# Performance work log

Hardware: AMD Instinct MI355X
Metric: run time of the kernel (lower is better)

## Reference

```python
import jax, jax.numpy as jnp
import numpy as np

B, S, HID = 2, 2048, 2048
NH, NKV, HD = 16, 4, 128  # num_heads, num_kv_heads, head_dim; kqv_size = NH*HD = 2048
KV_DIM = NKV * HD  # 512


def setup_inputs() -> dict:
    key = jax.random.key(0)
    ks = jax.random.split(key, 7)
    sc = 0.02
    return {
        "hidden_states": jax.random.normal(ks[0], (B, S, HID), dtype=jnp.float32),
        "Wq": jax.random.normal(ks[1], (NH * HD, HID), dtype=jnp.float32) * sc,
        "Wk": jax.random.normal(ks[2], (KV_DIM, HID), dtype=jnp.float32) * sc,
        "Wv": jax.random.normal(ks[3], (KV_DIM, HID), dtype=jnp.float32) * sc,
        "Wo": jax.random.normal(ks[4], (HID, NH * HD), dtype=jnp.float32) * sc,
        "bo": jnp.zeros((HID,), dtype=jnp.float32),
    }


def reference(hidden_states, Wq, Wk, Wv, Wo, bo):
    b, s, _ = hidden_states.shape
    # projections (nn.Linear: x @ W.T), no bias on q/k/v
    q = (hidden_states @ Wq.T).reshape(b, s, NH, HD).transpose(0, 2, 1, 3)   # [B,NH,S,HD]
    k = (hidden_states @ Wk.T).reshape(b, s, NKV, HD).transpose(0, 2, 1, 3)  # [B,NKV,S,HD]
    v = (hidden_states @ Wv.T).reshape(b, s, NKV, HD).transpose(0, 2, 1, 3)
    # GQA: query head h uses kv head h // (NH // NKV)
    g = NH // NKV
    k_rep = jnp.repeat(k, g, axis=1)  # [B,NH,S,HD]
    v_rep = jnp.repeat(v, g, axis=1)
    # float32 upcast, NO 1/sqrt(d) scaling (GPT-Neo style)
    qf = q.astype(jnp.float32)
    kf = k_rep.astype(jnp.float32)
    scores = jnp.einsum("bhqd,bhkd->bhqk", qf, kf)  # [B,NH,S,S]
    causal = jnp.tril(jnp.ones((s, s), dtype=bool))[None, None]
    neg = jnp.finfo(scores.dtype).min
    scores = jnp.where(causal, scores, neg)
    attn = jax.nn.softmax(scores, axis=-1).astype(v.dtype)  # dropout p=0 (eval)
    out = jnp.einsum("bhqk,bhkd->bhqd", attn, v_rep)         # [B,NH,S,HD]
    out = out.transpose(0, 2, 1, 3).reshape(b, s, NH * HD)
    return out @ Wo.T + bo
```

## Files before the change

### kernel.cpp

```cpp
#include <hip/hip_runtime.h>

typedef _Float16 f16;
typedef __attribute__((ext_vector_type(4))) _Float16 f16x4;
typedef __attribute__((ext_vector_type(8))) _Float16 f16x8;
typedef __attribute__((ext_vector_type(4))) float f32x4;

#define NB 2
#define NS 2048
#define NHID 2048
#define N_H 16
#define N_KV 4
#define N_HD 128

__device__ __forceinline__ void gload16(void* lds, const void* g) {
  __builtin_amdgcn_global_load_lds(
      (const __attribute__((address_space(1))) unsigned int*)g,
      (__attribute__((address_space(3))) unsigned int*)lds, 16, 0, 0);
}

__global__ __launch_bounds__(256) void cvt_all(
    const float* __restrict__ hs, const float* __restrict__ Wq,
    const float* __restrict__ Wk, const float* __restrict__ Wv,
    const float* __restrict__ Wo, f16* __restrict__ Xh,
    f16* __restrict__ Wqkv, f16* __restrict__ Woh) {
  int i = blockIdx.x * 256 + threadIdx.x;
  const float* src;
  f16* dst;
  int j;
  if (i < 2097152)      { src = hs; dst = Xh;             j = i; }
  else if (i < 3145728) { src = Wq; dst = Wqkv;           j = i - 2097152; }
  else if (i < 3407872) { src = Wk; dst = Wqkv + 4194304; j = i - 3145728; }
  else if (i < 3670016) { src = Wv; dst = Wqkv + 5242880; j = i - 3407872; }
  else                  { src = Wo; dst = Woh;            j = i - 3670016; }
  const float4 v = reinterpret_cast<const float4*>(src)[j];
  f16x4 o = {(f16)v.x, (f16)v.y, (f16)v.z, (f16)v.w};
  reinterpret_cast<f16x4*>(dst)[j] = o;
}

__global__ __launch_bounds__(512, 2) void gemm_qkv(
    const f16* __restrict__ A, const f16* __restrict__ Bm,
    f16* __restrict__ q_out, f16* __restrict__ k_out, f16* __restrict__ v_out) {
  constexpr int K = 2048;
  __shared__ f16 lds[2][28672];
  const int t = threadIdx.x;
  const int l = t & 63, w = t >> 6;
  const int g = l >> 4, l15 = l & 15;
  const int wr = w >> 2, wc = w & 3;
  const int orig = blockIdx.x;
  const int x = orig & 7, loc = orig >> 3;
  const int mb = (x & 3) * 4 + (loc & 3);
  const int nb = (x >> 2) * 8 + (loc >> 2);
  const f16* Ab = A + (size_t)(mb * 256) * K;
  const f16* Bb = Bm + (size_t)(nb * 192) * K;

  const int rA = ((t >> 5) << 3) | (t & 7);
  const int cA = (t >> 3) & 3;
  const int t2 = t & 255;
  const int rB2 = ((t2 >> 5) << 3) | (t2 & 7);
  const int cB2 = (t2 >> 3) & 3;

  auto stage = [&](int kt) {
    f16* buf = lds[kt & 1];
#pragma unroll
    for (int h = 0; h < 2; ++h) {
#pragma unroll
      for (int gi = 0; gi < 2; ++gi)
        gload16(buf + h * 8192 + gi * 4096 + w * 512,
                Ab + (size_t)(gi * 128 + rA) * K + kt * 64 + h * 32 + cA * 8);
      gload16(buf + 16384 + h * 6144 + w * 512,
              Bb + (size_t)rA * K + kt * 64 + h * 32 + cA * 8);
      if (t < 256)
        gload16(buf + 16384 + h * 6144 + 4096 + w * 512,
                Bb + (size_t)(128 + rB2) * K + kt * 64 + h * 32 + cB2 * 8);
    }
  };
  const int fragoff = ((l15 >> 3) << 8) + (g << 6) + ((l15 & 7) << 3);

  f32x4 acc[8][3] = {};

  stage(0);
  asm volatile("s_waitcnt vmcnt(0)" ::: "memory");
  __builtin_amdgcn_s_barrier();

  for (int kt = 0; kt < 32; ++kt) {
    if (kt + 1 < 32) stage(kt + 1);
    const f16* buf = lds[kt & 1];
#pragma unroll
    for (int h = 0; h < 2; ++h) {
      f16x8 af[8], bf[3];
#pragma unroll
      for (int mi = 0; mi < 8; ++mi)
        af[mi] = *reinterpret_cast<const f16x8*>(buf + h * 8192 + (wr * 128 + mi * 16) * 32 + fragoff);
#pragma unroll
      for (int ni = 0; ni < 3; ++ni)
        bf[ni] = *reinterpret_cast<const f16x8*>(buf + 16384 + h * 6144 + (wc * 48 + ni * 16) * 32 + fragoff);
      __builtin_amdgcn_s_setprio(1);
#pragma unroll
      for (int mi = 0; mi < 8; ++mi)
#pragma unroll
        for (int ni = 0; ni < 3; ++ni)
          acc[mi][ni] = __builtin_amdgcn_mfma_f32_16x16x32_f16(af[mi], bf[ni], acc[mi][ni], 0, 0, 0);
      __builtin_amdgcn_s_setprio(0);
    }
    if (kt + 1 < 32) asm volatile("s_waitcnt vmcnt(0)" ::: "memory");
    __builtin_amdgcn_s_barrier();
  }

#pragma unroll
  for (int mi = 0; mi < 8; ++mi) {
    int m0 = mb * 256 + wr * 128 + mi * 16 + 4 * g;
#pragma unroll
    for (int ni = 0; ni < 3; ++ni) {
      int n = nb * 192 + wc * 48 + ni * 16 + l15;
#pragma unroll
      for (int r = 0; r < 4; ++r) {
        int mm = m0 + r;
        float val = acc[mi][ni][r];
        int b = mm >> 11, s = mm & (NS - 1);
        if (n < 2048) {
          int h = n >> 7, d = n & 127;
          q_out[(((size_t)(b * N_H + h)) * NS + s) * N_HD + d] = (f16)val;
        } else if (n < 2560) {
          int n2 = n - 2048, kvh = n2 >> 7, d = n2 & 127;
          k_out[(((size_t)(b * N_KV + kvh)) * NS + s) * N_HD + d] = (f16)val;
        } else {
          int n3 = n - 2560, kvh = n3 >> 7, d = n3 & 127;
          v_out[(((size_t)(b * N_KV + kvh)) * NS + s) * N_HD + d] = (f16)val;
        }
      }
    }
  }
}

template <int MREP, int MODE>
__global__ __launch_bounds__(512, 2) void gemm8(
    const f16* __restrict__ A, const f16* __restrict__ Bm, const int K,
    float* __restrict__ f_out, const float* __restrict__ bias) {
  constexpr int BM = MREP * 32;
  constexpr int GA = BM / 128;
  constexpr int G = GA + 2;
  constexpr int NPH = (MREP == 8) ? 2 : 1;
  constexpr int ATILE = BM * 32;
  constexpr int BTILE = 256 * 32;
  constexpr int BUF = ATILE + BTILE;
  __shared__ f16 lds[4 * BUF];

  const int t = threadIdx.x;
  const int l = t & 63, w = t >> 6;
  const int g = l >> 4, l15 = l & 15;
  const int wr = w >> 2, wc = w & 3;
  const int orig = blockIdx.x;
  const int x = orig & 7, loc = orig >> 3;
  int mb, nb;
  mb = (x & 3) * 8 + (loc & 7); nb = (x >> 2) * 4 + (loc >> 3);
  const int NT = K >> 5;

  const f16* Aorig = A + (size_t)(mb * BM) * K;
  const f16* Borig = Bm + (size_t)(nb * 256) * K;

  size_t offA[GA], offB[2];
#pragma unroll
  for (int gi = 0; gi < GA; ++gi) {
    int beta = gi * 8192 + t * 16;
    int r = ((beta >> 9) << 3) | ((beta >> 4) & 7);
    int c = (beta >> 7) & 3;
    offA[gi] = (size_t)r * K + c * 8;
  }
#pragma unroll
  for (int gj = 0; gj < 2; ++gj) {
    int beta = gj * 8192 + t * 16;
    int r = ((beta >> 9) << 3) | ((beta >> 4) & 7);
    int c = (beta >> 7) & 3;
    offB[gj] = (size_t)r * K + c * 8;
  }

  auto stage = [&](int kt, int gi) {
    f16* bufbase = lds + (kt & 3) * BUF;
    if (gi < GA) {
      gload16(bufbase + gi * 4096 + w * 512, Aorig + offA[gi] + kt * 32);
    } else {
      int gj = gi - GA;
      gload16(bufbase + ATILE + gj * 4096 + w * 512, Borig + offB[gj] + kt * 32);
    }
  };
  const int fragoff = ((l15 >> 3) << 8) + (g << 6) + ((l15 & 7) << 3);
  auto readA = [&](int kt, int mi) -> f16x8 {
    int R0 = wr * (MREP * 16) + mi * 16;
    return *reinterpret_cast<const f16x8*>(lds + (kt & 3) * BUF + R0 * 32 + fragoff);
  };
  auto readB = [&](int kt, int ni) -> f16x8 {
    int R0 = wc * 64 + ni * 16;
    return *reinterpret_cast<const f16x8*>(lds + (kt & 3) * BUF + ATILE + R0 * 32 + fragoff);
  };

  f32x4 acc[MREP][4] = {};

#pragma unroll
  for (int pt = 0; pt < 3; ++pt)
#pragma unroll
    for (int gi = 0; gi < G; ++gi) stage(pt, gi);
  asm volatile("s_waitcnt vmcnt(6)" ::: "memory");
  __builtin_amdgcn_s_barrier();

  f16x8 bf[4];
  for (int kt = 0; kt < NT; ++kt) {
    const bool dostage = (kt + 3 < NT);
#pragma unroll
    for (int ph = 0; ph < NPH; ++ph) {
      f16x8 af[4];
#pragma unroll
      for (int mi = 0; mi < 4; ++mi) af[mi] = readA(kt, ph * 4 + mi);
      if (ph == 0) {
#pragma unroll
        for (int ni = 0; ni < 4; ++ni) bf[ni] = readB(kt, ni);
      }
      if (dostage) {
        stage(kt + 3, 0);
        stage(kt + 3, 1);
        stage(kt + 3, 2);
      }
      if (ph == NPH - 1) {
        if (kt + 3 < NT)      asm volatile("s_waitcnt vmcnt(6)" ::: "memory");
        else if (kt + 2 < NT) asm volatile("s_waitcnt vmcnt(3)" ::: "memory");
        else if (kt + 1 < NT) asm volatile("s_waitcnt vmcnt(0)" ::: "memory");
      }
      __builtin_amdgcn_s_barrier();
      asm volatile("s_waitcnt lgkmcnt(0)" ::: "memory");
      __builtin_amdgcn_s_setprio(1);
#pragma unroll
      for (int mi = 0; mi < 4; ++mi)
#pragma unroll
        for (int ni = 0; ni < 4; ++ni)
          acc[ph * 4 + mi][ni] =
              __builtin_amdgcn_mfma_f32_16x16x32_f16(af[mi], bf[ni], acc[ph * 4 + mi][ni], 0, 0, 0);
      __builtin_amdgcn_s_setprio(0);
      __builtin_amdgcn_s_barrier();
    }
  }

#pragma unroll
  for (int mi = 0; mi < MREP; ++mi) {
    int m0 = mb * BM + wr * (MREP * 16) + mi * 16 + 4 * g;
#pragma unroll
    for (int ni = 0; ni < 4; ++ni) {
      int n = nb * 256 + wc * 64 + ni * 16 + l15;
#pragma unroll
      for (int r = 0; r < 4; ++r) {
        f_out[(size_t)(m0 + r) * NHID + n] = acc[mi][ni][r] + bias[n];
      }
    }
  }
}

__global__ __launch_bounds__(256) void transpose_v(const f16* __restrict__ V,
                                                   f16* __restrict__ Vt) {
  __shared__ f16 tt[64][72];
  int s0 = blockIdx.x * 64, d0 = blockIdx.y * 64, bk = blockIdx.z;
  const f16* Vp = V + (size_t)bk * NS * N_HD;
  f16* Vtp = Vt + (size_t)bk * N_HD * NS;
  int tid = threadIdx.x;
#pragma unroll
  for (int it = 0; it < 2; ++it) {
    int c = it * 256 + tid;
    int sr = c >> 3, dc = (c & 7) * 8;
    f16x8 v = *reinterpret_cast<const f16x8*>(Vp + (size_t)(s0 + sr) * N_HD + d0 + dc);
#pragma unroll
    for (int j = 0; j < 8; ++j) tt[dc + j][sr] = v[j];
  }
  __syncthreads();
#pragma unroll
  for (int it = 0; it < 2; ++it) {
    int c = it * 256 + tid;
    int dr = c >> 3, sc = (c & 7) * 8;
    f16x8 o;
#pragma unroll
    for (int j = 0; j < 8; ++j) o[j] = tt[dr][sc + j];
    *reinterpret_cast<f16x8*>(Vtp + (size_t)(d0 + dr) * NS + s0 + sc) = o;
  }
}

__device__ __forceinline__ void stage_kv(const f16* __restrict__ Kp,
                                         const f16* __restrict__ Vp,
                                         f16* Kl, f16* Vl, int kt, int w, int l) {
#pragma unroll
  for (int it = 0; it < 4; ++it) {
    int cb = (it * 4 + w) * 64;
    int c = cb + l;
    int krow = c >> 4, pch = c & 15;
    int sch = (pch & 8) | ((pch ^ krow) & 7);
    gload16(Kl + cb * 8, Kp + (size_t)(kt * 64 + krow) * N_HD + sch * 8);
  }
#pragma unroll
  for (int it = 0; it < 4; ++it) {
    int cb = (it * 4 + w) * 64;
    int c = cb + l;
    int drow = c >> 3, pch = c & 7;
    int sch = (pch ^ drow) & 7;
    gload16(Vl + cb * 8, Vp + (size_t)drow * NS + kt * 64 + sch * 8);
  }
}

__device__ __forceinline__ void attn_step(
    const f16x8* qf, f32x4* oacc, float* mrow, float* lrow, int q0, int kt,
    const f16* Kl, const f16* Vl, f16* Pw, int g, int l15, bool diag) {
  f32x4 sacc[4];
#pragma unroll
  for (int nt = 0; nt < 4; ++nt) {
    f32x4 z = {0.f, 0.f, 0.f, 0.f};
#pragma unroll
    for (int ks = 0; ks < 4; ++ks) {
      int kr = nt * 16 + l15;
      int ch = ks * 4 + g;
      int sw = (ch & 8) | ((ch ^ kr) & 7);
      f16x8 kf = *reinterpret_cast<const f16x8*>(Kl + kr * 128 + sw * 8);
      z = __builtin_amdgcn_mfma_f32_16x16x32_f16(qf[ks], kf, z, 0, 0, 0);
    }
    sacc[nt] = z;
  }

  float p[4][4];
#pragma unroll
  for (int r = 0; r < 4; ++r) {
    int qg = q0 + r;
    float m = -3.0e38f;
#pragma unroll
    for (int nt = 0; nt < 4; ++nt) {
      float sv = sacc[nt][r];
      if (diag) {
        int kg = kt * 64 + nt * 16 + l15;
        if (kg > qg) sv = -3.0e38f;
      }
      p[nt][r] = sv;
      m = fmaxf(m, sv);
    }
#pragma unroll
    for (int off = 8; off >= 1; off >>= 1) m = fmaxf(m, __shfl_xor(m, off));
    float m2 = fmaxf(mrow[r], m);
    float alpha = __builtin_amdgcn_exp2f(mrow[r] - m2);
    mrow[r] = m2;
    lrow[r] *= alpha;
#pragma unroll
    for (int nt = 0; nt < 4; ++nt)
      p[nt][r] = __builtin_amdgcn_exp2f(p[nt][r] - m2);
#pragma unroll
    for (int dt = 0; dt < 8; ++dt) oacc[dt][r] *= alpha;
  }

#pragma unroll
  for (int nt = 0; nt < 4; ++nt)
#pragma unroll
    for (int r = 0; r < 4; ++r) {
      int ql = 4 * g + r;
      int kp = nt * 16 + l15;
      int ch = kp >> 3;
      int idx = ql * 64 + (ch ^ (ql & 7)) * 8 + (kp & 7);
      Pw[idx] = (f16)p[nt][r];
    }
  asm volatile("s_waitcnt lgkmcnt(0)" ::: "memory");
  __builtin_amdgcn_sched_barrier(0);

  f16x8 pa[2];
#pragma unroll
  for (int ks2 = 0; ks2 < 2; ++ks2) {
    int ch = ks2 * 4 + g;
    pa[ks2] = *reinterpret_cast<const f16x8*>(&Pw[l15 * 64 + (ch ^ (l15 & 7)) * 8]);
  }
  const f16x8 ones = {(f16)1.f, (f16)1.f, (f16)1.f, (f16)1.f,
                      (f16)1.f, (f16)1.f, (f16)1.f, (f16)1.f};
  f32x4 lacc = {0.f, 0.f, 0.f, 0.f};
#pragma unroll
  for (int ks2 = 0; ks2 < 2; ++ks2)
    lacc = __builtin_amdgcn_mfma_f32_16x16x32_f16(pa[ks2], ones, lacc, 0, 0, 0);
#pragma unroll
  for (int dt = 0; dt < 8; ++dt)
#pragma unroll
    for (int ks2 = 0; ks2 < 2; ++ks2) {
      int d = dt * 16 + l15;
      int ch = ks2 * 4 + g;
      f16x8 vf = *reinterpret_cast<const f16x8*>(Vl + d * 64 + (ch ^ (d & 7)) * 8);
      oacc[dt] = __builtin_amdgcn_mfma_f32_16x16x32_f16(pa[ks2], vf, oacc[dt], 0, 0, 0);
    }
#pragma unroll
  for (int r = 0; r < 4; ++r) lrow[r] += lacc[r];
}

__global__ __launch_bounds__(256, 2) void attn_kernel(
    const f16* __restrict__ Q, const f16* __restrict__ K,
    const f16* __restrict__ Vt, f16* __restrict__ O) {
  __shared__ f16 Klds[2][64 * 128];
  __shared__ f16 Vlds[2][128 * 64];
  __shared__ f16 Plds[4][16 * 64];
  const int t = threadIdx.x, l = t & 63, w = t >> 6;
  const int g = l >> 4, l15 = l & 15;
  const int orig = blockIdx.x;
  const int x = orig & 7, loc = orig >> 3;
  const int b = x >> 2, kvh = x & 3;
  const int h = kvh * 4 + (loc & 3);
  const int pi = loc >> 2;
  const int qtA = pi, qtB = 31 - pi;
  const f16* Qp = Q + ((size_t)(b * N_H + h)) * NS * N_HD;
  const f16* Kp = K + ((size_t)(b * N_KV + kvh)) * NS * N_HD;
  const f16* Vp = Vt + ((size_t)(b * N_KV + kvh)) * N_HD * NS;

  const f16 l2e = (f16)1.44269504f;
  f16x8 qfA[4], qfB[4];
  const int qrA = qtA * 64 + w * 16 + l15;
  const int qrB = qtB * 64 + w * 16 + l15;
#pragma unroll
  for (int ks = 0; ks < 4; ++ks) {
    qfA[ks] = *reinterpret_cast<const f16x8*>(Qp + (size_t)qrA * N_HD + ks * 32 + g * 8);
    qfB[ks] = *reinterpret_cast<const f16x8*>(Qp + (size_t)qrB * N_HD + ks * 32 + g * 8);
#pragma unroll
    for (int j = 0; j < 8; ++j) { qfA[ks][j] *= l2e; qfB[ks][j] *= l2e; }
  }

  f32x4 oA[8] = {}, oB[8] = {};
  float mA[4], lAr[4], mB[4], lBr[4];
#pragma unroll
  for (int r = 0; r < 4; ++r) {
    mA[r] = -3.0e38f; lAr[r] = 0.f;
    mB[r] = -3.0e38f; lBr[r] = 0.f;
  }
  const int q0A = qtA * 64 + w * 16 + 4 * g;
  const int q0B = qtB * 64 + w * 16 + 4 * g;

  const int nkt = qtB + 1;
  stage_kv(Kp, Vp, Klds[0], Vlds[0], 0, w, l);
  asm volatile("s_waitcnt vmcnt(0)" ::: "memory");
  __syncthreads();
  int cur = 0;
  for (int kt = 0; kt < nkt; ++kt) {
    if (kt + 1 < nkt)
      stage_kv(Kp, Vp, Klds[cur ^ 1], Vlds[cur ^ 1], kt + 1, w, l);
    attn_step(qfB, oB, mB, lBr, q0B, kt, Klds[cur], Vlds[cur], Plds[w], g, l15, kt == qtB);
    if (kt <= qtA)
      attn_step(qfA, oA, mA, lAr, q0A, kt, Klds[cur], Vlds[cur], Plds[w], g, l15, kt == qtA);
    asm volatile("s_waitcnt vmcnt(0)" ::: "memory");
    __syncthreads();
    cur ^= 1;
  }

#pragma unroll
  for (int r = 0; r < 4; ++r) {
    float invB = 1.0f / lBr[r];
    f16* orowB = O + (size_t)(b * NS + q0B + r) * NHID + h * N_HD;
#pragma unroll
    for (int dt = 0; dt < 8; ++dt) orowB[dt * 16 + l15] = (f16)(oB[dt][r] * invB);
    float invA = 1.0f / lAr[r];
    f16* orowA = O + (size_t)(b * NS + q0A + r) * NHID + h * N_HD;
#pragma unroll
    for (int dt = 0; dt < 8; ++dt) orowA[dt * 16 + l15] = (f16)(oA[dt][r] * invA);
  }
}

extern "C" void kernel_launch(void* const* d_in, const int* in_sizes, int n_in,
                              void* d_out, int out_size, void* d_ws, size_t ws_size,
                              hipStream_t stream) {
  const float* hs = (const float*)d_in[0];
  const float* Wq = (const float*)d_in[1];
  const float* Wk = (const float*)d_in[2];
  const float* Wv = (const float*)d_in[3];
  const float* Wo = (const float*)d_in[4];
  const float* bo = (const float*)d_in[5];
  float* out = (float*)d_out;

  char* ws = (char*)d_ws;
  f16* Xh   = (f16*)(ws);
  f16* Wqkv = (f16*)(ws + 16777216);
  f16* Woh  = (f16*)(ws + 29360128);
  f16* Qb   = (f16*)(ws + 37748736);
  f16* Kb   = (f16*)(ws + 54525952);
  f16* Vb   = (f16*)(ws + 58720256);
  f16* Vtb  = (f16*)(ws + 62914560);
  f16* Ob   = Xh;

  cvt_all<<<18432, 256, 0, stream>>>(hs, Wq, Wk, Wv, Wo, Xh, Wqkv, Woh);
  gemm_qkv<<<256, 512, 0, stream>>>(Xh, Wqkv, Qb, Kb, Vb);
  transpose_v<<<dim3(32, 2, 8), 256, 0, stream>>>(Vb, Vtb);
  attn_kernel<<<512, 256, 0, stream>>>(Qb, Kb, Vtb, Ob);
  gemm8<4, 1><<<256, 512, 0, stream>>>(Ob, Woh, 2048, out, bo);
}
```

Baseline: 216.1 us.

## Compute transposed attention scores to keep P in registers, skipping LDS round-trip

The attention step now computes S^T (K as the A operand, Q as B), so each lane owns one query row. The probabilities can then feed the PV MFMA directly as 16x16x16 B operands without being staged through LDS. This removes the per-step P write/read to shared memory, the lgkmcnt wait and the row-max shuffles, and simplifies the row statistics to scalars. The QKV GEMM also staggers which k-half each wave reads first to spread LDS bank traffic, and the output GEMM drops its unused multi-phase path. The trade-off is smaller 16x16x16 MFMAs and f16x4 V reads in place of the wider x32 instructions.

```diff
diff --git a/kernel.cpp b/kernel.cpp
--- a/kernel.cpp
+++ b/kernel.cpp
@@ -86,7 +86,8 @@
     if (kt + 1 < 32) stage(kt + 1);
     const f16* buf = lds[kt & 1];
 #pragma unroll
-    for (int h = 0; h < 2; ++h) {
+    for (int hi = 0; hi < 2; ++hi) {
+      const int h = hi ^ (w & 1);
       f16x8 af[8], bf[3];
 #pragma unroll
       for (int mi = 0; mi < 8; ++mi)
@@ -132,14 +133,13 @@
   }
 }
 
-template <int MREP, int MODE>
+template <int MREP>
 __global__ __launch_bounds__(512, 2) void gemm8(
     const f16* __restrict__ A, const f16* __restrict__ Bm, const int K,
     float* __restrict__ f_out, const float* __restrict__ bias) {
   constexpr int BM = MREP * 32;
   constexpr int GA = BM / 128;
   constexpr int G = GA + 2;
-  constexpr int NPH = (MREP == 8) ? 2 : 1;
   constexpr int ATILE = BM * 32;
   constexpr int BTILE = 256 * 32;
   constexpr int BUF = ATILE + BTILE;
@@ -151,8 +151,8 @@
   const int wr = w >> 2, wc = w & 3;
   const int orig = blockIdx.x;
   const int x = orig & 7, loc = orig >> 3;
-  int mb, nb;
-  mb = (x & 3) * 8 + (loc & 7); nb = (x >> 2) * 4 + (loc >> 3);
+  const int mb = (x & 3) * 8 + (loc & 7);
+  const int nb = (x >> 2) * 4 + (loc >> 3);
   const int NT = K >> 5;
 
   const f16* Aorig = A + (size_t)(mb * BM) * K;
@@ -202,40 +202,32 @@
   asm volatile("s_waitcnt vmcnt(6)" ::: "memory");
   __builtin_amdgcn_s_barrier();
 
-  f16x8 bf[4];
   for (int kt = 0; kt < NT; ++kt) {
-    const bool dostage = (kt + 3 < NT);
-#pragma unroll
-    for (int ph = 0; ph < NPH; ++ph) {
-      f16x8 af[4];
-#pragma unroll
-      for (int mi = 0; mi < 4; ++mi) af[mi] = readA(kt, ph * 4 + mi);
-      if (ph == 0) {
-#pragma unroll
-        for (int ni = 0; ni < 4; ++ni) bf[ni] = readB(kt, ni);
-      }
-      if (dostage) {
-        stage(kt + 3, 0);
-        stage(kt + 3, 1);
-        stage(kt + 3, 2);
-      }
-      if (ph == NPH - 1) {
-        if (kt + 3 < NT)      asm volatile("s_waitcnt vmcnt(6)" ::: "memory");
-        else if (kt + 2 < NT) asm volatile("s_waitcnt vmcnt(3)" ::: "memory");
-        else if (kt + 1 < NT) asm volatile("s_waitcnt vmcnt(0)" ::: "memory");
-      }
-      __builtin_amdgcn_s_barrier();
-      asm volatile("s_waitcnt lgkmcnt(0)" ::: "memory");
-      __builtin_amdgcn_s_setprio(1);
-#pragma unroll
-      for (int mi = 0; mi < 4; ++mi)
-#pragma unroll
-        for (int ni = 0; ni < 4; ++ni)
-          acc[ph * 4 + mi][ni] =
-              __builtin_amdgcn_mfma_f32_16x16x32_f16(af[mi], bf[ni], acc[ph * 4 + mi][ni], 0, 0, 0);
-      __builtin_amdgcn_s_setprio(0);
-      __builtin_amdgcn_s_barrier();
-    }
+    f16x8 af[4], bf[4];
+#pragma unroll
+    for (int mi = 0; mi < 4; ++mi) af[mi] = readA(kt, mi);
+#pragma unroll
+    for (int ni = 0; ni < 4; ++ni) bf[ni] = readB(kt, ni);
+    if (kt + 3 < NT) {
+      stage(kt + 3, 0);
+      stage(kt + 3, 1);
+      stage(kt + 3, 2);
+      asm volatile("s_waitcnt vmcnt(6)" ::: "memory");
+    } else if (kt + 2 < NT) {
+      asm volatile("s_waitcnt vmcnt(3)" ::: "memory");
+    } else if (kt + 1 < NT) {
+      asm volatile("s_waitcnt vmcnt(0)" ::: "memory");
+    }
+    __builtin_amdgcn_s_barrier();
+    asm volatile("s_waitcnt lgkmcnt(0)" ::: "memory");
+    __builtin_amdgcn_s_setprio(1);
+#pragma unroll
+    for (int mi = 0; mi < 4; ++mi)
+#pragma unroll
+      for (int ni = 0; ni < 4; ++ni)
+        acc[mi][ni] = __builtin_amdgcn_mfma_f32_16x16x32_f16(af[mi], bf[ni], acc[mi][ni], 0, 0, 0);
+    __builtin_amdgcn_s_setprio(0);
+    __builtin_amdgcn_s_barrier();
   }
 
 #pragma unroll
@@ -245,9 +237,8 @@
     for (int ni = 0; ni < 4; ++ni) {
       int n = nb * 256 + wc * 64 + ni * 16 + l15;
 #pragma unroll
-      for (int r = 0; r < 4; ++r) {
+      for (int r = 0; r < 4; ++r)
         f_out[(size_t)(m0 + r) * NHID + n] = acc[mi][ni][r] + bias[n];
-      }
     }
   }
 }
@@ -301,8 +292,8 @@
 }
 
 __device__ __forceinline__ void attn_step(
-    const f16x8* qf, f32x4* oacc, float* mrow, float* lrow, int q0, int kt,
-    const f16* Kl, const f16* Vl, f16* Pw, int g, int l15, bool diag) {
+    const f16x8* qf, f32x4* oacc, float& mrow, float& lrow, int qg, int kbase,
+    const f16* Kl, const f16* Vl, int g, int l15, bool diag) {
   f32x4 sacc[4];
 #pragma unroll
   for (int nt = 0; nt < 4; ++nt) {
@@ -313,75 +304,62 @@
       int ch = ks * 4 + g;
       int sw = (ch & 8) | ((ch ^ kr) & 7);
       f16x8 kf = *reinterpret_cast<const f16x8*>(Kl + kr * 128 + sw * 8);
-      z = __builtin_amdgcn_mfma_f32_16x16x32_f16(qf[ks], kf, z, 0, 0, 0);
+      z = __builtin_amdgcn_mfma_f32_16x16x32_f16(kf, qf[ks], z, 0, 0, 0);
     }
     sacc[nt] = z;
   }
 
-  float p[4][4];
-#pragma unroll
-  for (int r = 0; r < 4; ++r) {
-    int qg = q0 + r;
-    float m = -3.0e38f;
+  float pm[4][4];
+  float m = -3.0e38f;
+#pragma unroll
+  for (int nt = 0; nt < 4; ++nt)
+#pragma unroll
+    for (int r = 0; r < 4; ++r) {
+      float sv = sacc[nt][r];
+      if (diag && (kbase + nt * 16 + 4 * g + r > qg)) sv = -3.0e38f;
+      pm[nt][r] = sv;
+      m = fmaxf(m, sv);
+    }
+  m = fmaxf(m, __shfl_xor(m, 16));
+  m = fmaxf(m, __shfl_xor(m, 32));
+  float m2 = fmaxf(mrow, m);
+  float alpha = __builtin_amdgcn_exp2f(mrow - m2);
+  mrow = m2;
+
+  f16x4 p4[4];
+#pragma unroll
+  for (int nt = 0; nt < 4; ++nt) {
+    f16x4 q4 = {(f16)__builtin_amdgcn_exp2f(pm[nt][0] - m2),
+                (f16)__builtin_amdgcn_exp2f(pm[nt][1] - m2),
+                (f16)__builtin_amdgcn_exp2f(pm[nt][2] - m2),
+                (f16)__builtin_amdgcn_exp2f(pm[nt][3] - m2)};
+    p4[nt] = q4;
+  }
+
+  const f16x4 ones = {(f16)1.f, (f16)1.f, (f16)1.f, (f16)1.f};
+  f32x4 lacc = {0.f, 0.f, 0.f, 0.f};
+#pragma unroll
+  for (int nt = 0; nt < 4; ++nt)
+    lacc = __builtin_amdgcn_mfma_f32_16x16x16f16(ones, p4[nt], lacc, 0, 0, 0);
+  lrow = lrow * alpha + lacc[0];
+
+#pragma unroll
+  for (int dt = 0; dt < 8; ++dt) {
+    oacc[dt][0] *= alpha; oacc[dt][1] *= alpha;
+    oacc[dt][2] *= alpha; oacc[dt][3] *= alpha;
+  }
+
+#pragma unroll
+  for (int dt = 0; dt < 8; ++dt) {
+    int d = dt * 16 + l15;
 #pragma unroll
     for (int nt = 0; nt < 4; ++nt) {
-      float sv = sacc[nt][r];
-      if (diag) {
-        int kg = kt * 64 + nt * 16 + l15;
-        if (kg > qg) sv = -3.0e38f;
-      }
-      p[nt][r] = sv;
-      m = fmaxf(m, sv);
-    }
-#pragma unroll
-    for (int off = 8; off >= 1; off >>= 1) m = fmaxf(m, __shfl_xor(m, off));
-    float m2 = fmaxf(mrow[r], m);
-    float alpha = __builtin_amdgcn_exp2f(mrow[r] - m2);
-    mrow[r] = m2;
-    lrow[r] *= alpha;
-#pragma unroll
-    for (int nt = 0; nt < 4; ++nt)
-      p[nt][r] = __builtin_amdgcn_exp2f(p[nt][r] - m2);
-#pragma unroll
-    for (int dt = 0; dt < 8; ++dt) oacc[dt][r] *= alpha;
-  }
-
-#pragma unroll
-  for (int nt = 0; nt < 4; ++nt)
-#pragma unroll
-    for (int r = 0; r < 4; ++r) {
-      int ql = 4 * g + r;
-      int kp = nt * 16 + l15;
-      int ch = kp >> 3;
-      int idx = ql * 64 + (ch ^ (ql & 7)) * 8 + (kp & 7);
-      Pw[idx] = (f16)p[nt][r];
-    }
-  asm volatile("s_waitcnt lgkmcnt(0)" ::: "memory");
-  __builtin_amdgcn_sched_barrier(0);
-
-  f16x8 pa[2];
-#pragma unroll
-  for (int ks2 = 0; ks2 < 2; ++ks2) {
-    int ch = ks2 * 4 + g;
-    pa[ks2] = *reinterpret_cast<const f16x8*>(&Pw[l15 * 64 + (ch ^ (l15 & 7)) * 8]);
-  }
-  const f16x8 ones = {(f16)1.f, (f16)1.f, (f16)1.f, (f16)1.f,
-                      (f16)1.f, (f16)1.f, (f16)1.f, (f16)1.f};
-  f32x4 lacc = {0.f, 0.f, 0.f, 0.f};
-#pragma unroll
-  for (int ks2 = 0; ks2 < 2; ++ks2)
-    lacc = __builtin_amdgcn_mfma_f32_16x16x32_f16(pa[ks2], ones, lacc, 0, 0, 0);
-#pragma unroll
-  for (int dt = 0; dt < 8; ++dt)
-#pragma unroll
-    for (int ks2 = 0; ks2 < 2; ++ks2) {
-      int d = dt * 16 + l15;
-      int ch = ks2 * 4 + g;
-      f16x8 vf = *reinterpret_cast<const f16x8*>(Vl + d * 64 + (ch ^ (d & 7)) * 8);
-      oacc[dt] = __builtin_amdgcn_mfma_f32_16x16x32_f16(pa[ks2], vf, oacc[dt], 0, 0, 0);
-    }
-#pragma unroll
-  for (int r = 0; r < 4; ++r) lrow[r] += lacc[r];
+      int ch = 2 * nt + (g >> 1);
+      int sw = (ch ^ (d & 7)) & 7;
+      f16x4 vf = *reinterpret_cast<const f16x4*>(Vl + d * 64 + sw * 8 + 4 * (g & 1));
+      oacc[dt] = __builtin_amdgcn_mfma_f32_16x16x16f16(vf, p4[nt], oacc[dt], 0, 0, 0);
+    }
+  }
 }
 
 __global__ __launch_bounds__(256, 2) void attn_kernel(
@@ -389,7 +367,6 @@
     const f16* __restrict__ Vt, f16* __restrict__ O) {
   __shared__ f16 Klds[2][64 * 128];
   __shared__ f16 Vlds[2][128 * 64];
-  __shared__ f16 Plds[4][16 * 64];
   const int t = threadIdx.x, l = t & 63, w = t >> 6;
   const int g = l >> 4, l15 = l & 15;
   const int orig = blockIdx.x;
@@ -404,25 +381,18 @@
 
   const f16 l2e = (f16)1.44269504f;
   f16x8 qfA[4], qfB[4];
-  const int qrA = qtA * 64 + w * 16 + l15;
-  const int qrB = qtB * 64 + w * 16 + l15;
+  const int qgA = qtA * 64 + w * 16 + l15;
+  const int qgB = qtB * 64 + w * 16 + l15;
 #pragma unroll
   for (int ks = 0; ks < 4; ++ks) {
-    qfA[ks] = *reinterpret_cast<const f16x8*>(Qp + (size_t)qrA * N_HD + ks * 32 + g * 8);
-    qfB[ks] = *reinterpret_cast<const f16x8*>(Qp + (size_t)qrB * N_HD + ks * 32 + g * 8);
+    qfA[ks] = *reinterpret_cast<const f16x8*>(Qp + (size_t)qgA * N_HD + ks * 32 + g * 8);
+    qfB[ks] = *reinterpret_cast<const f16x8*>(Qp + (size_t)qgB * N_HD + ks * 32 + g * 8);
 #pragma unroll
     for (int j = 0; j < 8; ++j) { qfA[ks][j] *= l2e; qfB[ks][j] *= l2e; }
   }
 
   f32x4 oA[8] = {}, oB[8] = {};
-  float mA[4], lAr[4], mB[4], lBr[4];
-#pragma unroll
-  for (int r = 0; r < 4; ++r) {
-    mA[r] = -3.0e38f; lAr[r] = 0.f;
-    mB[r] = -3.0e38f; lBr[r] = 0.f;
-  }
-  const int q0A = qtA * 64 + w * 16 + 4 * g;
-  const int q0B = qtB * 64 + w * 16 + 4 * g;
+  float mA = -3.0e38f, lA = 0.f, mB = -3.0e38f, lB = 0.f;
 
   const int nkt = qtB + 1;
   stage_kv(Kp, Vp, Klds[0], Vlds[0], 0, w, l);
@@ -432,24 +402,29 @@
   for (int kt = 0; kt < nkt; ++kt) {
     if (kt + 1 < nkt)
       stage_kv(Kp, Vp, Klds[cur ^ 1], Vlds[cur ^ 1], kt + 1, w, l);
-    attn_step(qfB, oB, mB, lBr, q0B, kt, Klds[cur], Vlds[cur], Plds[w], g, l15, kt == qtB);
+    attn_step(qfB, oB, mB, lB, qgB, kt * 64, Klds[cur], Vlds[cur], g, l15, kt == qtB);
     if (kt <= qtA)
-      attn_step(qfA, oA, mA, lAr, q0A, kt, Klds[cur], Vlds[cur], Plds[w], g, l15, kt == qtA);
+      attn_step(qfA, oA, mA, lA, qgA, kt * 64, Klds[cur], Vlds[cur], g, l15, kt == qtA);
     asm volatile("s_waitcnt vmcnt(0)" ::: "memory");
     __syncthreads();
     cur ^= 1;
   }
 
-#pragma unroll
-  for (int r = 0; r < 4; ++r) {
-    float invB = 1.0f / lBr[r];
-    f16* orowB = O + (size_t)(b * NS + q0B + r) * NHID + h * N_HD;
-#pragma unroll
-    for (int dt = 0; dt < 8; ++dt) orowB[dt * 16 + l15] = (f16)(oB[dt][r] * invB);
-    float invA = 1.0f / lAr[r];
-    f16* orowA = O + (size_t)(b * NS + q0A + r) * NHID + h * N_HD;
-#pragma unroll
-    for (int dt = 0; dt < 8; ++dt) orowA[dt * 16 + l15] = (f16)(oA[dt][r] * invA);
+  float invB = 1.0f / lB;
+  f16* orowB = O + (size_t)(b * NS + qgB) * NHID + h * N_HD;
+#pragma unroll
+  for (int dt = 0; dt < 8; ++dt) {
+    f16x4 o4 = {(f16)(oB[dt][0] * invB), (f16)(oB[dt][1] * invB),
+                (f16)(oB[dt][2] * invB), (f16)(oB[dt][3] * invB)};
+    *reinterpret_cast<f16x4*>(orowB + dt * 16 + 4 * g) = o4;
+  }
+  float invA = 1.0f / lA;
+  f16* orowA = O + (size_t)(b * NS + qgA) * NHID + h * N_HD;
+#pragma unroll
+  for (int dt = 0; dt < 8; ++dt) {
+    f16x4 o4 = {(f16)(oA[dt][0] * invA), (f16)(oA[dt][1] * invA),
+                (f16)(oA[dt][2] * invA), (f16)(oA[dt][3] * invA)};
+    *reinterpret_cast<f16x4*>(orowA + dt * 16 + 4 * g) = o4;
   }
 }
 
@@ -478,5 +453,5 @@
   gemm_qkv<<<256, 512, 0, stream>>>(Xh, Wqkv, Qb, Kb, Vb);
   transpose_v<<<dim3(32, 2, 8), 256, 0, stream>>>(Vb, Vtb);
   attn_kernel<<<512, 256, 0, stream>>>(Qb, Kb, Vtb, Ob);
-  gemm8<4, 1><<<256, 512, 0, stream>>>(Ob, Woh, 2048, out, bo);
-}
+  gemm8<4><<<256, 512, 0, stream>>>(Ob, Woh, 2048, out, bo);
+}
```

New measurement: 294.2 us. +36.1%, slower.

## Retile QKV GEMM to 256x256 blocks with finer-grained pipelined staging

Applied to the files above, without the earlier changes.

The QKV projection GEMM moves from 256x192 tiles on 256 blocks to 256x256 tiles on 192 blocks, which raises MFMA work per LDS load. Global-to-LDS staging is split into quarter-tile chunks issued inside four sub-phases per k-tile, so loads overlap with MFMA work instead of waiting for a full vmcnt(0) each iteration. The output GEMM is simplified by removing the unused MODE/NPH template path. Using 192 blocks instead of 256 may leave some CUs idle, and the bigger LDS footprint with deeper waits could reduce occupancy.

```diff
diff --git a/kernel.cpp b/kernel.cpp
--- a/kernel.cpp
+++ b/kernel.cpp
@@ -41,7 +41,8 @@
     const f16* __restrict__ A, const f16* __restrict__ Bm,
     f16* __restrict__ q_out, f16* __restrict__ k_out, f16* __restrict__ v_out) {
   constexpr int K = 2048;
-  __shared__ f16 lds[2][28672];
+  constexpr int NT = 32;
+  __shared__ f16 lds[2][32768];
   const int t = threadIdx.x;
   const int l = t & 63, w = t >> 6;
   const int g = l >> 4, l15 = l & 15;
@@ -49,69 +50,97 @@
   const int orig = blockIdx.x;
   const int x = orig & 7, loc = orig >> 3;
   const int mb = (x & 3) * 4 + (loc & 3);
-  const int nb = (x >> 2) * 8 + (loc >> 2);
+  const int nb = (x >> 2) * 6 + (loc >> 2);
   const f16* Ab = A + (size_t)(mb * 256) * K;
-  const f16* Bb = Bm + (size_t)(nb * 192) * K;
-
-  const int rA = ((t >> 5) << 3) | (t & 7);
-  const int cA = (t >> 3) & 3;
-  const int t2 = t & 255;
-  const int rB2 = ((t2 >> 5) << 3) | (t2 & 7);
-  const int cB2 = (t2 >> 3) & 3;
-
-  auto stage = [&](int kt) {
-    f16* buf = lds[kt & 1];
-#pragma unroll
-    for (int h = 0; h < 2; ++h) {
-#pragma unroll
-      for (int gi = 0; gi < 2; ++gi)
-        gload16(buf + h * 8192 + gi * 4096 + w * 512,
-                Ab + (size_t)(gi * 128 + rA) * K + kt * 64 + h * 32 + cA * 8);
-      gload16(buf + 16384 + h * 6144 + w * 512,
-              Bb + (size_t)rA * K + kt * 64 + h * 32 + cA * 8);
-      if (t < 256)
-        gload16(buf + 16384 + h * 6144 + 4096 + w * 512,
-                Bb + (size_t)(128 + rB2) * K + kt * 64 + h * 32 + cB2 * 8);
-    }
-  };
+  const f16* Bb = Bm + (size_t)(nb * 256) * K;
+
+  const int rr = ((t >> 5) << 3) | (t & 7);
+  const int cc = (t >> 3) & 3;
+
+  auto stageA = [&](int tile, int h) {
+    f16* dstbase = lds[tile & 1] + h * 8192;
+    size_t so = (size_t)rr * K + tile * 64 + h * 32 + cc * 8;
+#pragma unroll
+    for (int gi = 0; gi < 2; ++gi)
+      gload16(dstbase + gi * 4096 + w * 512, Ab + so + (size_t)(gi * 128) * K);
+  };
+  auto stageB = [&](int tile, int h) {
+    f16* dstbase = lds[tile & 1] + 16384 + h * 8192;
+    size_t so = (size_t)rr * K + tile * 64 + h * 32 + cc * 8;
+#pragma unroll
+    for (int gi = 0; gi < 2; ++gi)
+      gload16(dstbase + gi * 4096 + w * 512, Bb + so + (size_t)(gi * 128) * K);
+  };
+  auto stage_n = [&](int n) {
+    if (n >= 4 * NT) return;
+    int tile = n >> 2, j = n & 3;
+    if (j < 2) stageB(tile, j);
+    else       stageA(tile, j - 2);
+  };
+
   const int fragoff = ((l15 >> 3) << 8) + (g << 6) + ((l15 & 7) << 3);
-
-  f32x4 acc[8][3] = {};
-
-  stage(0);
-  asm volatile("s_waitcnt vmcnt(0)" ::: "memory");
+  auto readA = [&](int tile, int mr, int ks) -> f16x8 {
+    return *reinterpret_cast<const f16x8*>(
+        lds[tile & 1] + ks * 8192 + (wr * 128 + mr * 16) * 32 + fragoff);
+  };
+  auto readB = [&](int tile, int ni, int ks) -> f16x8 {
+    return *reinterpret_cast<const f16x8*>(
+        lds[tile & 1] + 16384 + ks * 8192 + (wc * 64 + ni * 16) * 32 + fragoff);
+  };
+
+  f32x4 acc[8][4] = {};
+
+#pragma unroll
+  for (int n = 0; n < 6; ++n) stage_n(n);
+  asm volatile("s_waitcnt vmcnt(4)" ::: "memory");
   __builtin_amdgcn_s_barrier();
 
-  for (int kt = 0; kt < 32; ++kt) {
-    if (kt + 1 < 32) stage(kt + 1);
-    const f16* buf = lds[kt & 1];
-#pragma unroll
-    for (int h = 0; h < 2; ++h) {
-      f16x8 af[8], bf[3];
-#pragma unroll
-      for (int mi = 0; mi < 8; ++mi)
-        af[mi] = *reinterpret_cast<const f16x8*>(buf + h * 8192 + (wr * 128 + mi * 16) * 32 + fragoff);
-#pragma unroll
-      for (int ni = 0; ni < 3; ++ni)
-        bf[ni] = *reinterpret_cast<const f16x8*>(buf + 16384 + h * 6144 + (wc * 48 + ni * 16) * 32 + fragoff);
+  f16x8 bf[4][2];
+  for (int T = 0; T < NT; ++T) {
+#pragma unroll
+    for (int q = 0; q < 4; ++q) {
+      if (q == 0 && T > 0) {
+        if (T == NT - 1) asm volatile("s_waitcnt vmcnt(0)" ::: "memory");
+        else             asm volatile("s_waitcnt vmcnt(4)" ::: "memory");
+      }
+      f16x8 af[2][2];
+#pragma unroll
+      for (int i = 0; i < 2; ++i)
+#pragma unroll
+        for (int ks = 0; ks < 2; ++ks)
+          af[i][ks] = readA(T, 2 * q + i, ks);
+      if (q == 0) {
+#pragma unroll
+        for (int ni = 0; ni < 4; ++ni)
+#pragma unroll
+          for (int ks = 0; ks < 2; ++ks)
+            bf[ni][ks] = readB(T, ni, ks);
+      }
+      stage_n(T * 4 + q + 6);
+      if (q == 0) asm volatile("s_waitcnt lgkmcnt(8)" ::: "memory");
+      __builtin_amdgcn_s_barrier();
+      asm volatile("s_waitcnt lgkmcnt(0)" ::: "memory");
+      __builtin_amdgcn_sched_barrier(0);
       __builtin_amdgcn_s_setprio(1);
 #pragma unroll
-      for (int mi = 0; mi < 8; ++mi)
-#pragma unroll
-        for (int ni = 0; ni < 3; ++ni)
-          acc[mi][ni] = __builtin_amdgcn_mfma_f32_16x16x32_f16(af[mi], bf[ni], acc[mi][ni], 0, 0, 0);
+      for (int i = 0; i < 2; ++i)
+#pragma unroll
+        for (int ni = 0; ni < 4; ++ni)
+#pragma unroll
+          for (int ks = 0; ks < 2; ++ks)
+            acc[2 * q + i][ni] = __builtin_amdgcn_mfma_f32_16x16x32_f16(
+                af[i][ks], bf[ni][ks], acc[2 * q + i][ni], 0, 0, 0);
       __builtin_amdgcn_s_setprio(0);
-    }
-    if (kt + 1 < 32) asm volatile("s_waitcnt vmcnt(0)" ::: "memory");
-    __builtin_amdgcn_s_barrier();
+      __builtin_amdgcn_s_barrier();
+    }
   }
 
 #pragma unroll
   for (int mi = 0; mi < 8; ++mi) {
     int m0 = mb * 256 + wr * 128 + mi * 16 + 4 * g;
 #pragma unroll
-    for (int ni = 0; ni < 3; ++ni) {
-      int n = nb * 192 + wc * 48 + ni * 16 + l15;
+    for (int ni = 0; ni < 4; ++ni) {
+      int n = nb * 256 + wc * 64 + ni * 16 + l15;
 #pragma unroll
       for (int r = 0; r < 4; ++r) {
         int mm = m0 + r;
@@ -132,14 +161,13 @@
   }
 }
 
-template <int MREP, int MODE>
+template <int MREP>
 __global__ __launch_bounds__(512, 2) void gemm8(
     const f16* __restrict__ A, const f16* __restrict__ Bm, const int K,
     float* __restrict__ f_out, const float* __restrict__ bias) {
   constexpr int BM = MREP * 32;
   constexpr int GA = BM / 128;
   constexpr int G = GA + 2;
-  constexpr int NPH = (MREP == 8) ? 2 : 1;
   constexpr int ATILE = BM * 32;
   constexpr int BTILE = 256 * 32;
   constexpr int BUF = ATILE + BTILE;
@@ -151,8 +179,8 @@
   const int wr = w >> 2, wc = w & 3;
   const int orig = blockIdx.x;
   const int x = orig & 7, loc = orig >> 3;
-  int mb, nb;
-  mb = (x & 3) * 8 + (loc & 7); nb = (x >> 2) * 4 + (loc >> 3);
+  const int mb = (x & 3) * 8 + (loc & 7);
+  const int nb = (x >> 2) * 4 + (loc >> 3);
   const int NT = K >> 5;
 
   const f16* Aorig = A + (size_t)(mb * BM) * K;
@@ -202,40 +230,32 @@
   asm volatile("s_waitcnt vmcnt(6)" ::: "memory");
   __builtin_amdgcn_s_barrier();
 
-  f16x8 bf[4];
   for (int kt = 0; kt < NT; ++kt) {
-    const bool dostage = (kt + 3 < NT);
-#pragma unroll
-    for (int ph = 0; ph < NPH; ++ph) {
-      f16x8 af[4];
-#pragma unroll
-      for (int mi = 0; mi < 4; ++mi) af[mi] = readA(kt, ph * 4 + mi);
-      if (ph == 0) {
-#pragma unroll
-        for (int ni = 0; ni < 4; ++ni) bf[ni] = readB(kt, ni);
-      }
-      if (dostage) {
-        stage(kt + 3, 0);
-        stage(kt + 3, 1);
-        stage(kt + 3, 2);
-      }
-      if (ph == NPH - 1) {
-        if (kt + 3 < NT)      asm volatile("s_waitcnt vmcnt(6)" ::: "memory");
-        else if (kt + 2 < NT) asm volatile("s_waitcnt vmcnt(3)" ::: "memory");
-        else if (kt + 1 < NT) asm volatile("s_waitcnt vmcnt(0)" ::: "memory");
-      }
-      __builtin_amdgcn_s_barrier();
-      asm volatile("s_waitcnt lgkmcnt(0)" ::: "memory");
-      __builtin_amdgcn_s_setprio(1);
-#pragma unroll
-      for (int mi = 0; mi < 4; ++mi)
-#pragma unroll
-        for (int ni = 0; ni < 4; ++ni)
-          acc[ph * 4 + mi][ni] =
-              __builtin_amdgcn_mfma_f32_16x16x32_f16(af[mi], bf[ni], acc[ph * 4 + mi][ni], 0, 0, 0);
-      __builtin_amdgcn_s_setprio(0);
-      __builtin_amdgcn_s_barrier();
-    }
+    f16x8 af[4], bf[4];
+#pragma unroll
+    for (int mi = 0; mi < 4; ++mi) af[mi] = readA(kt, mi);
+#pragma unroll
+    for (int ni = 0; ni < 4; ++ni) bf[ni] = readB(kt, ni);
+    if (kt + 3 < NT) {
+      stage(kt + 3, 0);
+      stage(kt + 3, 1);
+      stage(kt + 3, 2);
+      asm volatile("s_waitcnt vmcnt(6)" ::: "memory");
+    } else if (kt + 2 < NT) {
+      asm volatile("s_waitcnt vmcnt(3)" ::: "memory");
+    } else if (kt + 1 < NT) {
+      asm volatile("s_waitcnt vmcnt(0)" ::: "memory");
+    }
+    __builtin_amdgcn_s_barrier();
+    asm volatile("s_waitcnt lgkmcnt(0)" ::: "memory");
+    __builtin_amdgcn_s_setprio(1);
+#pragma unroll
+    for (int mi = 0; mi < 4; ++mi)
+#pragma unroll
+      for (int ni = 0; ni < 4; ++ni)
+        acc[mi][ni] = __builtin_amdgcn_mfma_f32_16x16x32_f16(af[mi], bf[ni], acc[mi][ni], 0, 0, 0);
+    __builtin_amdgcn_s_setprio(0);
+    __builtin_amdgcn_s_barrier();
   }
 
 #pragma unroll
@@ -245,9 +265,8 @@
     for (int ni = 0; ni < 4; ++ni) {
       int n = nb * 256 + wc * 64 + ni * 16 + l15;
 #pragma unroll
-      for (int r = 0; r < 4; ++r) {
+      for (int r = 0; r < 4; ++r)
         f_out[(size_t)(m0 + r) * NHID + n] = acc[mi][ni][r] + bias[n];
-      }
     }
   }
 }
@@ -475,8 +494,8 @@
   f16* Ob   = Xh;
 
   cvt_all<<<18432, 256, 0, stream>>>(hs, Wq, Wk, Wv, Wo, Xh, Wqkv, Woh);
-  gemm_qkv<<<256, 512, 0, stream>>>(Xh, Wqkv, Qb, Kb, Vb);
+  gemm_qkv<<<192, 512, 0, stream>>>(Xh, Wqkv, Qb, Kb, Vb);
   transpose_v<<<dim3(32, 2, 8), 256, 0, stream>>>(Vb, Vtb);
   attn_kernel<<<512, 256, 0, stream>>>(Qb, Kb, Vtb, Ob);
-  gemm8<4, 1><<<256, 512, 0, stream>>>(Ob, Woh, 2048, out, bo);
-}
+  gemm8<4><<<256, 512, 0, stream>>>(Ob, Woh, 2048, out, bo);
+}
```

Measured after the change: 212.8 us. About the same (-1.5%).
